# Kernel tuning notes

Measured on AMD Instinct MI355X. Metric: run time of the kernel, lower is better.

The kernel has to match this reference:

```python
import jax, jax.numpy as jnp
import numpy as np

INPUT_SIZE, HIDDEN, OUT = 2, 32, 1

def setup_inputs() -> dict:
    key = jax.random.key(0)
    ks = jax.random.split(key, 8)
    B, T = 2048, 512
    s_ih = 1.0 / np.sqrt(HIDDEN)
    return {
        "x": jax.random.normal(ks[0], (B, T, INPUT_SIZE), dtype=jnp.float32),
        "W_ih": jax.random.uniform(ks[1], (4 * HIDDEN, INPUT_SIZE), minval=-s_ih, maxval=s_ih, dtype=jnp.float32),
        "W_hh": jax.random.uniform(ks[2], (4 * HIDDEN, HIDDEN), minval=-s_ih, maxval=s_ih, dtype=jnp.float32),
        "b_ih": jax.random.uniform(ks[3], (4 * HIDDEN,), minval=-s_ih, maxval=s_ih, dtype=jnp.float32),
        "b_hh": jax.random.uniform(ks[4], (4 * HIDDEN,), minval=-s_ih, maxval=s_ih, dtype=jnp.float32),
        "W_fc": jax.random.uniform(ks[5], (OUT, HIDDEN), minval=-s_ih, maxval=s_ih, dtype=jnp.float32),
        "b_fc": jax.random.uniform(ks[6], (OUT,), minval=-s_ih, maxval=s_ih, dtype=jnp.float32),
    }

def _lstm(x, W_ih, W_hh, b_ih, b_hh):
    # x: [B, T, I]; PyTorch gate order: i, f, g, o
    B, T, _ = x.shape
    H = W_hh.shape[1]
    # precompute input projections for all timesteps: [T, B, 4H]
    xp = jnp.einsum('bti,gi->tbg', x, W_ih) + (b_ih + b_hh)

    def step(carry, xp_t):
        h, c = carry
        gates = xp_t + h @ W_hh.T  # [B, 4H]
        i, f, g, o = jnp.split(gates, 4, axis=-1)
        i = jax.nn.sigmoid(i)
        f = jax.nn.sigmoid(f)
        g = jnp.tanh(g)
        o = jax.nn.sigmoid(o)
        c = f * c + i * g
        h = o * jnp.tanh(c)
        return (h, c), h

    h0 = jnp.zeros((B, H), dtype=x.dtype)
    c0 = jnp.zeros((B, H), dtype=x.dtype)
    _, hs = jax.lax.scan(step, (h0, c0), xp)  # hs: [T, B, H]
    return jnp.transpose(hs, (1, 0, 2))  # [B, T, H]

def reference(x, W_ih, W_hh, b_ih, b_hh, W_fc, b_fc):
    lstm_out = _lstm(x, W_ih, W_hh, b_ih, b_hh)  # [B, T, H]
    return lstm_out @ W_fc.T + b_fc  # [B, T, OUT]
```

## Files before the change

kernel.cpp:

```cpp
#include <hip/hip_runtime.h>


#define BB 2048
#define TT 512
#define HH 32
#define CHUNK 64
#define HROW 33

#define LOG2E 1.44269504088896340736f

typedef float v2f __attribute__((ext_vector_type(2)));
typedef float v4f __attribute__((ext_vector_type(4)));
typedef unsigned int v2u __attribute__((ext_vector_type(2)));

__device__ __forceinline__ float sigm2(float xs) {
    return __builtin_amdgcn_rcpf(1.0f + __builtin_amdgcn_exp2f(-xs));
}

__global__ __launch_bounds__(256, 2) void lstm_fused_kernel(
    const float* __restrict__ x,
    const float* __restrict__ W_ih,
    const float* __restrict__ W_hh,
    const float* __restrict__ b_ih,
    const float* __restrict__ b_hh,
    const float* __restrict__ W_fc,
    const float* __restrict__ b_fc,
    float* __restrict__ out)
{
    __shared__ float lds_x[4 * TT * 2];
    __shared__ float lds_h[4 * CHUNK * HROW];
    __shared__ __align__(16) float lds_bc[4][64];

    const int lane = threadIdx.x & 63;
    const int wv   = threadIdx.x >> 6;
    const int b    = blockIdx.x * 4 + wv;
    const bool low = (lane < 32);

    {
        const float4* xg = (const float4*)(x + (size_t)b * TT * 2);
        float4* xs = (float4*)(lds_x + wv * TT * 2);
        #pragma unroll
        for (int r = 0; r < 4; ++r) xs[r * 64 + lane] = xg[r * 64 + lane];
    }

    const int rlo = lane;
    const int rhi = lane + 64;
    const float sl = LOG2E;
    const float sh = low ? 2.0f * LOG2E : LOG2E;

    const v2f wihl = ((const v2f*)W_ih)[rlo] * sl;
    const v2f wihh = ((const v2f*)W_ih)[rhi] * sh;
    const float bl = (b_ih[rlo] + b_hh[rlo]) * sl;
    const float bh = (b_ih[rhi] + b_hh[rhi]) * sh;

    v2f wloq[HH / 2], whiq[HH / 2];
    #pragma unroll
    for (int k = 0; k < HH / 2; ++k) {
        wloq[k] = ((const v2f*)(W_hh + rlo * HH))[k] * sl;
        whiq[k] = ((const v2f*)(W_hh + rhi * HH))[k] * sh;
    }

    float wfc[HH];
    #pragma unroll
    for (int u = 0; u < HH; ++u) wfc[u] = W_fc[u];
    const float bfc = b_fc[0];

    const float Aa = low ?  4.0f * LOG2E : 1.0f;
    const float Bb = low ? -2.0f * LOG2E : 0.0f;

    float c = 0.0f;

    float* out_b = out + (size_t)b * TT;
    const v4f* xw4 = (const v4f*)(lds_x + wv * TT * 2);
    float* hb  = lds_h + wv * CHUNK * HROW;
    float* bcw = lds_bc[wv];
    const v4f* bcr = (const v4f*)bcw;

    bcw[lane] = 0.0f;

    const v2f binitL = {bl, 0.0f};
    const v2f binitH = {bh, 0.0f};

    float* wr = low ? (bcw + lane) : (hb + (lane - 32));
    const int winc = low ? 0 : HROW;

    #pragma unroll 1
    for (int ch = 0; ch < TT / CHUNK; ++ch) {
        #pragma unroll 1
        for (int uu = 0; uu < CHUNK; uu += 4) {
            v4f xq0 = xw4[(ch * CHUNK + uu) >> 1];
            v4f xq1 = xw4[((ch * CHUNK + uu) >> 1) + 1];

            #pragma unroll
            for (int s = 0; s < 4; ++s) {
                v4f hq[8];
                #pragma unroll
                for (int q = 0; q < 8; ++q) hq[q] = bcr[q];

                v2f xt;
                if      (s == 0) xt = (v2f){xq0.x, xq0.y};
                else if (s == 1) xt = (v2f){xq0.z, xq0.w};
                else if (s == 2) xt = (v2f){xq1.x, xq1.y};
                else             xt = (v2f){xq1.z, xq1.w};

                v2f aL0 = __builtin_elementwise_fma(xt, wihl, binitL);
                v2f aH0 = __builtin_elementwise_fma(xt, wihh, binitH);
                v2f aL1, aH1;

                #pragma unroll
                for (int k = 0; k < HH / 2; ++k) {
                    v2f hp = (k & 1)
                        ? __builtin_shufflevector(hq[k >> 1], hq[k >> 1], 2, 3)
                        : __builtin_shufflevector(hq[k >> 1], hq[k >> 1], 0, 1);
                    if (k < HH / 4) {
                        aL0 = __builtin_elementwise_fma(hp, wloq[k], aL0);
                        aH0 = __builtin_elementwise_fma(hp, whiq[k], aH0);
                    } else if (k == HH / 4) {
                        aL1 = hp * wloq[k];
                        aH1 = hp * whiq[k];
                    } else {
                        aL1 = __builtin_elementwise_fma(hp, wloq[k], aL1);
                        aH1 = __builtin_elementwise_fma(hp, whiq[k], aH1);
                    }
                }
                v2f aL = aL0 + aL1;
                v2f aH = aH0 + aH1;
                float glo = aL.x + aL.y;
                float ghi = aH.x + aH.y;

                float alo = sigm2(glo);
                float shi = sigm2(ghi);
                float ahi = fmaf(Aa, shi, Bb);

                v2u r1 = __builtin_amdgcn_permlane32_swap(
                    __float_as_uint(alo), __float_as_uint(alo), false, false);
                v2u r2 = __builtin_amdgcn_permlane32_swap(
                    __float_as_uint(ahi), __float_as_uint(ahi), false, false);
                float fv = __uint_as_float(r1.y);
                float iv = __uint_as_float(r1.x);
                float ov = __uint_as_float(r2.y);
                float gv = __uint_as_float(r2.x);

                float ig = iv * gv;
                c = fmaf(fv, c, ig);

                float rr  = sigm2(c);
                float ov2 = ov + ov;
                float hnew = fmaf(ov2, rr, -ov);

                *wr = hnew;
                wr += winc;
            }
        }

        wr -= winc * CHUNK;

        float acc = bfc;
        const float* row = hb + lane * HROW;
        #pragma unroll
        for (int u = 0; u < HH; ++u)
            acc = fmaf(row[u], wfc[u], acc);
        out_b[ch * CHUNK + lane] = acc;
    }
}

extern "C" void kernel_launch(void* const* d_in, const int* in_sizes, int n_in,
                              void* d_out, int out_size, void* d_ws, size_t ws_size,
                              hipStream_t stream) {
    const float* x    = (const float*)d_in[0];
    const float* W_ih = (const float*)d_in[1];
    const float* W_hh = (const float*)d_in[2];
    const float* b_ih = (const float*)d_in[3];
    const float* b_hh = (const float*)d_in[4];
    const float* W_fc = (const float*)d_in[5];
    const float* b_fc = (const float*)d_in[6];
    float* out = (float*)d_out;

    dim3 grid(BB / 4);
    dim3 block(256);
    lstm_fused_kernel<<<grid, block, 0, stream>>>(x, W_ih, W_hh, b_ih, b_hh,
                                                  W_fc, b_fc, out);
}
```

Baseline: 211.9 us.

## Map two batch elements per wavefront with each lane computing all four gates

Each wavefront now handles two batch elements, one per half-wave. Each lane computes all four gates for one hidden unit, which removes the permlane32 swaps. The grid is halved, and x is streamed from global memory with one-step-ahead prefetch instead of being staged in LDS. A ring of h rows in LDS serves both as the broadcast source and as FC input, with CHUNK reduced to 32. This doubles per-lane register pressure (launch bounds lowered to 1 block per SIMD pair) and halves the number of waves, trading latency hiding for fewer cross-lane ops and less LDS traffic.

```diff
diff --git a/kernel.cpp b/kernel.cpp
--- a/kernel.cpp
+++ b/kernel.cpp
@@ -4,20 +4,21 @@
 #define BB 2048
 #define TT 512
 #define HH 32
-#define CHUNK 64
-#define HROW 33
+#define CHUNK 32
+#define ROWF 36
+#define EPAD 4
+#define WSTRIDE (2 * CHUNK * ROWF + EPAD)
 
 #define LOG2E 1.44269504088896340736f
 
 typedef float v2f __attribute__((ext_vector_type(2)));
 typedef float v4f __attribute__((ext_vector_type(4)));
-typedef unsigned int v2u __attribute__((ext_vector_type(2)));
 
 __device__ __forceinline__ float sigm2(float xs) {
     return __builtin_amdgcn_rcpf(1.0f + __builtin_amdgcn_exp2f(-xs));
 }
 
-__global__ __launch_bounds__(256, 2) void lstm_fused_kernel(
+__global__ __launch_bounds__(256, 1) void lstm_fused_kernel(
     const float* __restrict__ x,
     const float* __restrict__ W_ih,
     const float* __restrict__ W_hh,
@@ -27,37 +28,34 @@
     const float* __restrict__ b_fc,
     float* __restrict__ out)
 {
-    __shared__ float lds_x[4 * TT * 2];
-    __shared__ float lds_h[4 * CHUNK * HROW];
-    __shared__ __align__(16) float lds_bc[4][64];
+    __shared__ __align__(16) float lds_h[4][WSTRIDE];
 
     const int lane = threadIdx.x & 63;
     const int wv   = threadIdx.x >> 6;
-    const int b    = blockIdx.x * 4 + wv;
-    const bool low = (lane < 32);
+    const int elem = lane >> 5;
+    const int j    = lane & 31;
+    const int b    = blockIdx.x * 8 + wv * 2 + elem;
 
-    {
-        const float4* xg = (const float4*)(x + (size_t)b * TT * 2);
-        float4* xs = (float4*)(lds_x + wv * TT * 2);
-        #pragma unroll
-        for (int r = 0; r < 4; ++r) xs[r * 64 + lane] = xg[r * 64 + lane];
-    }
+    const int ri = j, rf = HH + j, rg = 2 * HH + j, ro = 3 * HH + j;
+    const float si = LOG2E;
+    const float sg = 2.0f * LOG2E;
 
-    const int rlo = lane;
-    const int rhi = lane + 64;
-    const float sl = LOG2E;
-    const float sh = low ? 2.0f * LOG2E : LOG2E;
+    const v2f wihI = ((const v2f*)W_ih)[ri] * si;
+    const v2f wihF = ((const v2f*)W_ih)[rf] * si;
+    const v2f wihG = ((const v2f*)W_ih)[rg] * sg;
+    const v2f wihO = ((const v2f*)W_ih)[ro] * si;
+    const float bI = (b_ih[ri] + b_hh[ri]) * si;
+    const float bF = (b_ih[rf] + b_hh[rf]) * si;
+    const float bG = (b_ih[rg] + b_hh[rg]) * sg;
+    const float bO = (b_ih[ro] + b_hh[ro]) * si;
 
-    const v2f wihl = ((const v2f*)W_ih)[rlo] * sl;
-    const v2f wihh = ((const v2f*)W_ih)[rhi] * sh;
-    const float bl = (b_ih[rlo] + b_hh[rlo]) * sl;
-    const float bh = (b_ih[rhi] + b_hh[rhi]) * sh;
-
-    v2f wloq[HH / 2], whiq[HH / 2];
+    v2f wI[HH / 2], wF[HH / 2], wG[HH / 2], wO[HH / 2];
     #pragma unroll
     for (int k = 0; k < HH / 2; ++k) {
-        wloq[k] = ((const v2f*)(W_hh + rlo * HH))[k] * sl;
-        whiq[k] = ((const v2f*)(W_hh + rhi * HH))[k] * sh;
+        wI[k] = ((const v2f*)(W_hh + ri * HH))[k] * si;
+        wF[k] = ((const v2f*)(W_hh + rf * HH))[k] * si;
+        wG[k] = ((const v2f*)(W_hh + rg * HH))[k] * sg;
+        wO[k] = ((const v2f*)(W_hh + ro * HH))[k] * si;
     }
 
     float wfc[HH];
@@ -65,37 +63,38 @@
     for (int u = 0; u < HH; ++u) wfc[u] = W_fc[u];
     const float bfc = b_fc[0];
 
-    const float Aa = low ?  4.0f * LOG2E : 1.0f;
-    const float Bb = low ? -2.0f * LOG2E : 0.0f;
-
     float c = 0.0f;
 
-    float* out_b = out + (size_t)b * TT;
-    const v4f* xw4 = (const v4f*)(lds_x + wv * TT * 2);
-    float* hb  = lds_h + wv * CHUNK * HROW;
-    float* bcw = lds_bc[wv];
-    const v4f* bcr = (const v4f*)bcw;
+    float* hb = &lds_h[wv][elem * (CHUNK * ROWF + EPAD)];
+    float* wr = hb + j;
+    const float* rd = hb + (CHUNK - 1) * ROWF;
 
-    bcw[lane] = 0.0f;
+    wr[(CHUNK - 1) * ROWF] = 0.0f;
 
-    const v2f binitL = {bl, 0.0f};
-    const v2f binitH = {bh, 0.0f};
+    const float* xb = x + (size_t)b * (TT * 2);
+    float* outp = out + (size_t)b * TT + j;
 
-    float* wr = low ? (bcw + lane) : (hb + (lane - 32));
-    const int winc = low ? 0 : HROW;
+    v4f xq0 = *(const v4f*)(xb);
+    v4f xq1 = *(const v4f*)(xb + 4);
+
+    const v2f bI2 = {bI, 0.0f}, bF2 = {bF, 0.0f};
+    const v2f bG2 = {bG, 0.0f}, bO2 = {bO, 0.0f};
 
     #pragma unroll 1
     for (int ch = 0; ch < TT / CHUNK; ++ch) {
         #pragma unroll 1
         for (int uu = 0; uu < CHUNK; uu += 4) {
-            v4f xq0 = xw4[(ch * CHUNK + uu) >> 1];
-            v4f xq1 = xw4[((ch * CHUNK + uu) >> 1) + 1];
+            const int t = ch * CHUNK + uu;
+            const float* xnx = (t + 4 < TT) ? (xb + (t + 4) * 2) : xb;
+            v4f nxq0 = *(const v4f*)(xnx);
+            v4f nxq1 = *(const v4f*)(xnx + 4);
 
             #pragma unroll
             for (int s = 0; s < 4; ++s) {
                 v4f hq[8];
+                const v4f* rq = (const v4f*)rd;
                 #pragma unroll
-                for (int q = 0; q < 8; ++q) hq[q] = bcr[q];
+                for (int q = 0; q < 8; ++q) hq[q] = rq[q];
 
                 v2f xt;
                 if      (s == 0) xt = (v2f){xq0.x, xq0.y};
@@ -103,9 +102,11 @@
                 else if (s == 2) xt = (v2f){xq1.x, xq1.y};
                 else             xt = (v2f){xq1.z, xq1.w};
 
-                v2f aL0 = __builtin_elementwise_fma(xt, wihl, binitL);
-                v2f aH0 = __builtin_elementwise_fma(xt, wihh, binitH);
-                v2f aL1, aH1;
+                v2f aI0 = __builtin_elementwise_fma(xt, wihI, bI2);
+                v2f aF0 = __builtin_elementwise_fma(xt, wihF, bF2);
+                v2f aG0 = __builtin_elementwise_fma(xt, wihG, bG2);
+                v2f aO0 = __builtin_elementwise_fma(xt, wihO, bO2);
+                v2f aI1, aF1, aG1, aO1;
 
                 #pragma unroll
                 for (int k = 0; k < HH / 2; ++k) {
@@ -113,54 +114,54 @@
                         ? __builtin_shufflevector(hq[k >> 1], hq[k >> 1], 2, 3)
                         : __builtin_shufflevector(hq[k >> 1], hq[k >> 1], 0, 1);
                     if (k < HH / 4) {
-                        aL0 = __builtin_elementwise_fma(hp, wloq[k], aL0);
-                        aH0 = __builtin_elementwise_fma(hp, whiq[k], aH0);
+                        aI0 = __builtin_elementwise_fma(hp, wI[k], aI0);
+                        aF0 = __builtin_elementwise_fma(hp, wF[k], aF0);
+                        aG0 = __builtin_elementwise_fma(hp, wG[k], aG0);
+                        aO0 = __builtin_elementwise_fma(hp, wO[k], aO0);
                     } else if (k == HH / 4) {
-                        aL1 = hp * wloq[k];
-                        aH1 = hp * whiq[k];
+                        aI1 = hp * wI[k]; aF1 = hp * wF[k];
+                        aG1 = hp * wG[k]; aO1 = hp * wO[k];
                     } else {
-                        aL1 = __builtin_elementwise_fma(hp, wloq[k], aL1);
-                        aH1 = __builtin_elementwise_fma(hp, whiq[k], aH1);
+                        aI1 = __builtin_elementwise_fma(hp, wI[k], aI1);
+                        aF1 = __builtin_elementwise_fma(hp, wF[k], aF1);
+                        aG1 = __builtin_elementwise_fma(hp, wG[k], aG1);
+                        aO1 = __builtin_elementwise_fma(hp, wO[k], aO1);
                     }
                 }
-                v2f aL = aL0 + aL1;
-                v2f aH = aH0 + aH1;
-                float glo = aL.x + aL.y;
-                float ghi = aH.x + aH.y;
+                v2f aI = aI0 + aI1, aF = aF0 + aF1;
+                v2f aG = aG0 + aG1, aO = aO0 + aO1;
+                float gi = aI.x + aI.y;
+                float gf = aF.x + aF.y;
+                float gg = aG.x + aG.y;
+                float go = aO.x + aO.y;
 
-                float alo = sigm2(glo);
-                float shi = sigm2(ghi);
-                float ahi = fmaf(Aa, shi, Bb);
+                float iv = sigm2(gi);
+                float fv = sigm2(gf);
+                float ov = sigm2(go);
+                float gv = fmaf(4.0f * LOG2E, sigm2(gg), -2.0f * LOG2E);
 
-                v2u r1 = __builtin_amdgcn_permlane32_swap(
-                    __float_as_uint(alo), __float_as_uint(alo), false, false);
-                v2u r2 = __builtin_amdgcn_permlane32_swap(
-                    __float_as_uint(ahi), __float_as_uint(ahi), false, false);
-                float fv = __uint_as_float(r1.y);
-                float iv = __uint_as_float(r1.x);
-                float ov = __uint_as_float(r2.y);
-                float gv = __uint_as_float(r2.x);
+                c = fmaf(fv, c, iv * gv);
 
-                float ig = iv * gv;
-                c = fmaf(fv, c, ig);
-
-                float rr  = sigm2(c);
-                float ov2 = ov + ov;
+                float rr   = sigm2(c);
+                float ov2  = ov + ov;
                 float hnew = fmaf(ov2, rr, -ov);
 
                 *wr = hnew;
-                wr += winc;
+                rd = wr - j;
+                wr += ROWF;
             }
+            xq0 = nxq0; xq1 = nxq1;
         }
 
-        wr -= winc * CHUNK;
+        wr -= CHUNK * ROWF;
 
         float acc = bfc;
-        const float* row = hb + lane * HROW;
+        const float* row = hb + j * ROWF;
         #pragma unroll
         for (int u = 0; u < HH; ++u)
             acc = fmaf(row[u], wfc[u], acc);
-        out_b[ch * CHUNK + lane] = acc;
+        *outp = acc;
+        outp += CHUNK;
     }
 }
 
@@ -176,7 +177,7 @@
     const float* b_fc = (const float*)d_in[6];
     float* out = (float*)d_out;
 
-    dim3 grid(BB / 4);
+    dim3 grid(BB / 8);
     dim3 block(256);
     lstm_fused_kernel<<<grid, block, 0, stream>>>(x, W_ih, W_hh, b_ih, b_hh,
                                                   W_fc, b_fc, out);
```

After: 205.5 us. 1.03x faster.
